# Optimization experiments

Measured on AMD Instinct MI355X. Metric: run time of the kernel, lower is better.

Reference implementation:

```python
import jax, jax.numpy as jnp
import numpy as np

TOP_K = 2  # num_experts_per_tok

def setup_inputs() -> dict:
    key = jax.random.key(0)
    ks = jax.random.split(key, 6)
    B, S, D, E, H = 4, 2048, 1024, 8, 4096
    x  = jax.random.normal(ks[0], (B, S, D), dtype=jnp.float32)
    Wg = jax.random.normal(ks[1], (D, E), dtype=jnp.float32) * 0.02
    W1 = jax.random.normal(ks[2], (E, D, H), dtype=jnp.float32) * 0.02
    b1 = jnp.zeros((E, H), dtype=jnp.float32)
    W2 = jax.random.normal(ks[3], (E, H, D), dtype=jnp.float32) * 0.02
    b2 = jnp.zeros((E, D), dtype=jnp.float32)
    return {"x": x, "Wg": Wg, "W1": W1, "b1": b1, "W2": W2, "b2": b2}

def reference(x, Wg, W1, b1, W2, b2):
    B, S, D = x.shape
    E = Wg.shape[1]
    xf = x.reshape(-1, D)                       # [T, D]
    T = xf.shape[0]
    logits = xf @ Wg                            # [T, E]
    probs = jax.nn.softmax(logits, axis=-1)
    weights, indices = jax.lax.top_k(probs, TOP_K)   # [T, K]
    # Dense combine weights: cw[t, e] = routing weight if e in top-k of t else 0.
    cw = jnp.zeros((T, E), dtype=x.dtype).at[jnp.arange(T)[:, None], indices].set(weights)
    out = jnp.zeros_like(xf)
    for e in range(E):  # small fixed expert count; per-expert GEMMs
        h = jax.nn.gelu(xf @ W1[e] + b1[e], approximate=False)  # [T, H]
        y = h @ W2[e] + b2[e]                                   # [T, D]
        out = out + y * cw[:, e:e + 1]
    return out.reshape(B, S, D)
```

## Files before the change

kernel.cpp:

```cpp
#include <hip/hip_runtime.h>
#include <hip/hip_bf16.h>
#include <stdint.h>

#define D_DIM 1024
#define E_NUM 8
#define H_DIM 4096

typedef __attribute__((ext_vector_type(8))) short short8;
typedef __attribute__((ext_vector_type(4))) short short4v;
typedef __attribute__((ext_vector_type(4))) unsigned short ushort4v;
typedef __attribute__((ext_vector_type(4))) float f32x4;

#define GLOBAL_AS __attribute__((address_space(1)))
#define LDS_AS __attribute__((address_space(3)))

__device__ __forceinline__ void async_load16(const void* g, void* l) {
    __builtin_amdgcn_global_load_lds((GLOBAL_AS void*)g, (LDS_AS void*)l, 16, 0, 0);
}

__device__ __forceinline__ float gelu_fast(float x) {
    float x3 = x * x * x;
    float z = 0.7978845608028654f * x + 0.0356774081363001f * x3;
    float u = __expf(-2.0f * fabsf(z));
    float t = __fdividef(1.0f - u, 1.0f + u);
    t = copysignf(t, z);
    return 0.5f * x * (1.0f + t);
}

__device__ __forceinline__ float b2f(short s) {
    union { float f; unsigned u; } x; x.u = ((unsigned)(unsigned short)s) << 16; return x.f;
}

__device__ __forceinline__ unsigned short f2b(float f) {
    union { __hip_bfloat16 h; unsigned short s; } u;
    u.h = __float2bfloat16(f);
    return u.s;
}

__global__ __launch_bounds__(256) void router_kernel(
    const float* __restrict__ x, const float* __restrict__ Wg,
    __hip_bfloat16* __restrict__ xb, int* __restrict__ epick,
    float* __restrict__ ewgt, int T) {
    int gwave = (int)((blockIdx.x * 256 + threadIdx.x) >> 6);
    int lane = threadIdx.x & 63;
    if (gwave >= T) return;
    const float* xr = x + (size_t)gwave * D_DIM;
    unsigned short* xbr = (unsigned short*)xb + (size_t)gwave * D_DIM;
    double acc[E_NUM];
#pragma unroll
    for (int e = 0; e < E_NUM; ++e) acc[e] = 0.0;
#pragma unroll
    for (int i = 0; i < D_DIM / 128; ++i) {
        int d = i * 128 + lane * 2;
        float2 xv = *(const float2*)(xr + d);
        unsigned pk = (unsigned)f2b(xv.x) | ((unsigned)f2b(xv.y) << 16);
        *(unsigned*)(xbr + d) = pk;
        const float4* wg0 = (const float4*)(Wg + (size_t)d * E_NUM);
        const float4* wg1 = (const float4*)(Wg + (size_t)(d + 1) * E_NUM);
        float4 wa = wg0[0], wb = wg0[1], wc = wg1[0], wd = wg1[1];
        double x0 = (double)xv.x, x1 = (double)xv.y;
        acc[0] += x0 * (double)wa.x + x1 * (double)wc.x;
        acc[1] += x0 * (double)wa.y + x1 * (double)wc.y;
        acc[2] += x0 * (double)wa.z + x1 * (double)wc.z;
        acc[3] += x0 * (double)wa.w + x1 * (double)wc.w;
        acc[4] += x0 * (double)wb.x + x1 * (double)wd.x;
        acc[5] += x0 * (double)wb.y + x1 * (double)wd.y;
        acc[6] += x0 * (double)wb.z + x1 * (double)wd.z;
        acc[7] += x0 * (double)wb.w + x1 * (double)wd.w;
    }
#pragma unroll
    for (int s = 32; s > 0; s >>= 1) {
#pragma unroll
        for (int e = 0; e < E_NUM; ++e) acc[e] += __shfl_xor(acc[e], s);
    }
    double mx = acc[0];
#pragma unroll
    for (int e = 1; e < E_NUM; ++e) mx = fmax(mx, acc[e]);
    double p[E_NUM]; double sum = 0.0;
#pragma unroll
    for (int e = 0; e < E_NUM; ++e) { p[e] = exp(acc[e] - mx); sum += p[e]; }
    int i0 = 0;
#pragma unroll
    for (int e = 1; e < E_NUM; ++e) if (p[e] > p[i0]) i0 = e;
    int i1 = (i0 == 0) ? 1 : 0;
#pragma unroll
    for (int e = 0; e < E_NUM; ++e) if (e != i0 && p[e] > p[i1]) i1 = e;
    if (lane == 0) {
        epick[gwave] = i0 | (i1 << 8);
        ewgt[2 * gwave]     = (float)(p[i0] / sum);
        ewgt[2 * gwave + 1] = (float)(p[i1] / sum);
    }
}

__global__ __launch_bounds__(256) void bucket_kernel(
    const int* __restrict__ epick, int* __restrict__ cnt,
    int* __restrict__ tok, int* __restrict__ eidx, int T) {
    __shared__ int lcnt[E_NUM];
    __shared__ int gbase[E_NUM];
    int b = blockIdx.x, tid = threadIdx.x;
    if (tid < E_NUM) lcnt[tid] = 0;
    __syncthreads();
    int t = b * 128 + (tid >> 1);
    int j = tid & 1;
    int e = (epick[t] >> (j * 8)) & 0xff;
    int li = atomicAdd(&lcnt[e], 1);
    __syncthreads();
    if (tid < E_NUM) gbase[tid] = atomicAdd(&cnt[tid], lcnt[tid]);
    __syncthreads();
    int slot = gbase[e] + li;
    tok[e * T + slot] = t;
    eidx[2 * t + j] = (e << 16) | slot;
}

__global__ void prefix_kernel(const int* __restrict__ cnt, int* __restrict__ base) {
    if (threadIdx.x == 0) {
        int a = 0;
#pragma unroll
        for (int e = 0; e < E_NUM; ++e) { base[e] = a; a += cnt[e]; }
    }
}

__global__ __launch_bounds__(256) void transpose_both_kernel(
    const float* __restrict__ W1, const float* __restrict__ W2,
    __hip_bfloat16* __restrict__ w1t, __hip_bfloat16* __restrict__ w2t) {
    __shared__ float tile[64][65];
    int e = blockIdx.z;
    int id = blockIdx.x;
    const float* src; unsigned short* dst; int R, C, r0, c0, perm;
    if (id < 1024) {
        R = D_DIM; C = H_DIM;
        r0 = (id >> 6) * 64; c0 = (id & 63) * 64;
        src = W1 + (size_t)e * D_DIM * H_DIM;
        dst = (unsigned short*)(w1t + (size_t)e * H_DIM * D_DIM);
        perm = 0;
    } else {
        id -= 1024;
        R = H_DIM; C = D_DIM;
        r0 = (id >> 4) * 64; c0 = (id & 15) * 64;
        src = W2 + (size_t)e * H_DIM * D_DIM;
        dst = (unsigned short*)(w2t + (size_t)e * D_DIM * H_DIM);
        perm = 1;
    }
    int tx = threadIdx.x, ty = threadIdx.y;
#pragma unroll
    for (int i = 0; i < 8; ++i) {
        int j = ty + i * 8;
        int sr = perm ? ((j & 3) * 16 + (j >> 2)) : j;
        float2 v = *(const float2*)(src + (size_t)(r0 + sr) * C + c0 + 2 * tx);
        tile[j][2 * tx] = v.x; tile[j][2 * tx + 1] = v.y;
    }
    __syncthreads();
#pragma unroll
    for (int i = 0; i < 8; ++i) {
        int cc = ty + i * 8;
        unsigned pk = (unsigned)f2b(tile[2 * tx][cc]) | ((unsigned)f2b(tile[2 * tx + 1][cc]) << 16);
        *(unsigned*)(dst + (size_t)(c0 + cc) * R + r0 + 2 * tx) = pk;
    }
}


__global__ __launch_bounds__(256) void gemm1_kernel(
    const __hip_bfloat16* __restrict__ xb,
    const __hip_bfloat16* __restrict__ w1t,
    const float* __restrict__ b1,
    const int* __restrict__ cnt, const int* __restrict__ base,
    const int* __restrict__ tok,
    __hip_bfloat16* __restrict__ hbuf,
    int T) {
    int e = blockIdx.z;
    int M = cnt[e];
    int m0 = blockIdx.y * 128;
    if (m0 >= M) return;
    int n0 = blockIdx.x * 128;
    const __hip_bfloat16* Bp = w1t + (size_t)e * H_DIM * D_DIM;

    __shared__ __align__(16) short sA[128 * 32];
    __shared__ __align__(16) short sB[128 * 32];
    __shared__ float sBias[128];
    char* sAc = (char*)sA; char* sBc = (char*)sB;

    int tid = threadIdx.x;
    int w = tid >> 6, lane = tid & 63;
    int wm = w >> 1, wn = w & 1;
    int q = lane >> 4, l4 = lane & 15;

    if (tid < 128) sBias[tid] = b1[e * H_DIM + n0 + tid];

    int kswz = ((lane & 3) ^ ((lane >> 3) & 3)) << 3;
    int r0 = w * 32 + (lane >> 2);
    int r1 = r0 + 16;
    int tA0 = tok[e * T + min(m0 + r0, M - 1)];
    int tA1 = tok[e * T + min(m0 + r1, M - 1)];
    const __hip_bfloat16* gA0 = xb + (size_t)tA0 * D_DIM + kswz;
    const __hip_bfloat16* gA1 = xb + (size_t)tA1 * D_DIM + kswz;
    const __hip_bfloat16* gB0 = Bp + (size_t)(n0 + r0) * D_DIM + kswz;
    const __hip_bfloat16* gB1 = Bp + (size_t)(n0 + r1) * D_DIM + kswz;
    char* lA0 = sAc + w * 2048 + lane * 16;
    char* lB0 = sBc + w * 2048 + lane * 16;
    char* lA1 = sAc + w * 2048 + 1024;
    char* lB1 = sBc + w * 2048 + 1024;

    f32x4 acc[4][4];
#pragma unroll
    for (int a = 0; a < 4; ++a)
#pragma unroll
        for (int b = 0; b < 4; ++b) acc[a][b] = (f32x4){0.f, 0.f, 0.f, 0.f};

    for (int kk = 0; kk < D_DIM; kk += 32) {
        async_load16(gA0 + kk, lA0);
        async_load16(gA1 + kk, lA1);
        async_load16(gB0 + kk, lB0);
        async_load16(gB1 + kk, lB1);
        __syncthreads();
        short8 aF[4], bF[4];
#pragma unroll
        for (int t = 0; t < 4; ++t) {
            int ra = wm * 64 + t * 16 + l4;
            aF[t] = *(const short8*)(sAc + ra * 64 + ((q ^ ((ra >> 1) & 3)) << 4));
            int rb = wn * 64 + t * 16 + l4;
            bF[t] = *(const short8*)(sBc + rb * 64 + ((q ^ ((rb >> 1) & 3)) << 4));
        }
#pragma unroll
        for (int tm = 0; tm < 4; ++tm)
#pragma unroll
            for (int tn = 0; tn < 4; ++tn)
                acc[tm][tn] = __builtin_amdgcn_mfma_f32_16x16x32_bf16(aF[tm], bF[tn], acc[tm][tn], 0, 0, 0);
        __syncthreads();
    }

    int sb = base[e];
    unsigned short* hs = (unsigned short*)hbuf;
#pragma unroll
    for (int tm = 0; tm < 4; ++tm) {
        int rbase = wm * 64 + tm * 16 + q * 4;
#pragma unroll
        for (int i = 0; i < 4; ++i) {
            int row = m0 + rbase + i;
            if (row < M) {
                size_t hrow = (size_t)(sb + row) * H_DIM;
                ushort4v pk;
#pragma unroll
                for (int tn = 0; tn < 4; ++tn) {
                    float v = acc[tm][tn][i] + sBias[wn * 64 + tn * 16 + l4];
                    pk[tn] = f2b(gelu_fast(v));
                }
                *(ushort4v*)(hs + hrow + n0 + wn * 64 + l4 * 4) = pk;
            }
        }
    }
}

__global__ __launch_bounds__(256) void gemm2_kernel(
    const __hip_bfloat16* __restrict__ hbuf,
    const __hip_bfloat16* __restrict__ w2t,
    const int* __restrict__ cnt, const int* __restrict__ base,
    __hip_bfloat16* __restrict__ ybuf,
    int T) {
    int e = blockIdx.z;
    int M = cnt[e];
    int m0 = blockIdx.y * 128;
    if (m0 >= M) return;
    int n0 = blockIdx.x * 128;
    int sb = base[e];
    const __hip_bfloat16* Bp = w2t + (size_t)e * D_DIM * H_DIM;

    __shared__ __align__(16) short sA[128 * 32];
    __shared__ __align__(16) short sB[128 * 32];
    char* sAc = (char*)sA; char* sBc = (char*)sB;

    int tid = threadIdx.x;
    int w = tid >> 6, lane = tid & 63;
    int wm = w >> 1, wn = w & 1;
    int q = lane >> 4, l4 = lane & 15;

    int kswz = ((lane & 3) ^ ((lane >> 3) & 3)) << 3;
    int r0 = w * 32 + (lane >> 2);
    int r1 = r0 + 16;
    const __hip_bfloat16* gA0 = hbuf + (size_t)(sb + min(m0 + r0, M - 1)) * H_DIM + kswz;
    const __hip_bfloat16* gA1 = hbuf + (size_t)(sb + min(m0 + r1, M - 1)) * H_DIM + kswz;
    const __hip_bfloat16* gB0 = Bp + (size_t)(n0 + r0) * H_DIM + kswz;
    const __hip_bfloat16* gB1 = Bp + (size_t)(n0 + r1) * H_DIM + kswz;
    char* lA0 = sAc + w * 2048 + lane * 16;
    char* lB0 = sBc + w * 2048 + lane * 16;
    char* lA1 = sAc + w * 2048 + 1024;
    char* lB1 = sBc + w * 2048 + 1024;

    f32x4 acc[4][4];
#pragma unroll
    for (int a = 0; a < 4; ++a)
#pragma unroll
        for (int b = 0; b < 4; ++b) acc[a][b] = (f32x4){0.f, 0.f, 0.f, 0.f};

    for (int kk = 0; kk < H_DIM; kk += 32) {
        async_load16(gA0 + kk, lA0);
        async_load16(gA1 + kk, lA1);
        async_load16(gB0 + kk, lB0);
        async_load16(gB1 + kk, lB1);
        __syncthreads();
        short8 aF[4], bF[4];
#pragma unroll
        for (int t = 0; t < 4; ++t) {
            int ra = wm * 64 + t * 16 + l4;
            aF[t] = *(const short8*)(sAc + ra * 64 + ((q ^ ((ra >> 1) & 3)) << 4));
            int rb = wn * 64 + t * 16 + l4;
            bF[t] = *(const short8*)(sBc + rb * 64 + ((q ^ ((rb >> 1) & 3)) << 4));
        }
#pragma unroll
        for (int tm = 0; tm < 4; ++tm)
#pragma unroll
            for (int tn = 0; tn < 4; ++tn)
                acc[tm][tn] = __builtin_amdgcn_mfma_f32_16x16x32_bf16(aF[tm], bF[tn], acc[tm][tn], 0, 0, 0);
        __syncthreads();
    }

    unsigned short* ys = (unsigned short*)ybuf;
#pragma unroll
    for (int tm = 0; tm < 4; ++tm) {
        int rbase = wm * 64 + tm * 16 + q * 4;
#pragma unroll
        for (int i = 0; i < 4; ++i) {
            int row = m0 + rbase + i;
            if (row < M) {
                size_t yrow = (size_t)(sb + row) * D_DIM;
                ushort4v pk;
#pragma unroll
                for (int tn = 0; tn < 4; ++tn) pk[tn] = f2b(acc[tm][tn][i]);
                *(ushort4v*)(ys + yrow + n0 + wn * 64 + l4 * 4) = pk;
            }
        }
    }
}

__global__ __launch_bounds__(256) void combine_kernel(
    const __hip_bfloat16* __restrict__ yb, const float* __restrict__ b2,
    const int* __restrict__ base, const int* __restrict__ eidx,
    const float* __restrict__ ewgt, float* __restrict__ out, int T) {
    int t = blockIdx.x, tid = threadIdx.x;
    int v0 = eidx[2 * t], v1 = eidx[2 * t + 1];
    float w0 = ewgt[2 * t], w1 = ewgt[2 * t + 1];
    int e0 = v0 >> 16, e1 = v1 >> 16;
    size_t g0 = (size_t)base[e0] + (v0 & 0xffff);
    size_t g1 = (size_t)base[e1] + (v1 & 0xffff);
    int c = tid * 4;
    int blk = c >> 6;
    int tt = (c >> 2) & 15;
    const short* ys = (const short*)yb;
    short4v a0 = *(const short4v*)(ys + g0 * D_DIM + c);
    short4v c0 = *(const short4v*)(ys + g1 * D_DIM + c);
    float s0[4] = { b2f(a0.x), b2f(a0.y), b2f(a0.z), b2f(a0.w) };
    float s1[4] = { b2f(c0.x), b2f(c0.y), b2f(c0.z), b2f(c0.w) };
    float* orow = out + (size_t)t * D_DIM;
#pragma unroll
    for (int s = 0; s < 4; ++s) {
        int oc = blk * 64 + s * 16 + tt;
        float o = w0 * (s0[s] + b2[(size_t)e0 * D_DIM + oc]) +
                  w1 * (s1[s] + b2[(size_t)e1 * D_DIM + oc]);
        orow[oc] = o;
    }
}

extern "C" void kernel_launch(void* const* d_in, const int* in_sizes, int n_in,
                              void* d_out, int out_size, void* d_ws, size_t ws_size,
                              hipStream_t stream) {
    const float* x  = (const float*)d_in[0];
    const float* Wg = (const float*)d_in[1];
    const float* W1 = (const float*)d_in[2];
    const float* b1 = (const float*)d_in[3];
    const float* W2 = (const float*)d_in[4];
    const float* b2 = (const float*)d_in[5];
    int T = in_sizes[0] / D_DIM;

    char* p = (char*)d_ws;
    int* cnt   = (int*)p;
    int* base  = (int*)(p + 256);
    int* tok   = (int*)(p + 512);
    int* eidx  = (int*)(p + 512 + 4ll * E_NUM * T);
    float* ewgt = (float*)(p + 512 + 4ll * E_NUM * T + 8ll * T);
    int* epick = (int*)(p + 512 + 4ll * E_NUM * T + 16ll * T);
    char* pb = p + 512 + 4ll * E_NUM * T + 20ll * T;
    __hip_bfloat16* xb  = (__hip_bfloat16*)pb;
    __hip_bfloat16* w1t = xb + (size_t)T * D_DIM;
    __hip_bfloat16* w2t = w1t + (size_t)E_NUM * H_DIM * D_DIM;
    __hip_bfloat16* hb  = w2t + (size_t)E_NUM * H_DIM * D_DIM;
    __hip_bfloat16* yb  = xb;

    hipMemsetAsync(cnt, 0, 256, stream);

    router_kernel<<<dim3((T + 3) / 4), 256, 0, stream>>>(x, Wg, xb, epick, ewgt, T);
    bucket_kernel<<<dim3(T / 128), 256, 0, stream>>>(epick, cnt, tok, eidx, T);
    prefix_kernel<<<1, 64, 0, stream>>>(cnt, base);
    transpose_both_kernel<<<dim3(2048, 1, E_NUM), dim3(32, 8), 0, stream>>>(W1, W2, w1t, w2t);
    gemm1_kernel<<<dim3(H_DIM / 128, T / 128, E_NUM), 256, 0, stream>>>(xb, w1t, b1, cnt, base, tok, hb, T);
    gemm2_kernel<<<dim3(D_DIM / 128, T / 128, E_NUM), 256, 0, stream>>>(hb, w2t, cnt, base, yb, T);
    combine_kernel<<<T, 256, 0, stream>>>(yb, b2, base, eidx, ewgt, (float*)d_out, T);
}
```

Baseline: 781.7 us.

## Compact expert tile work table and split-K the second expert GEMM

The prefix kernel now builds a compact table of (expert, row-block) pairs. Both GEMMs launch only over real tiles instead of a dense E×(T/128) grid where most blocks exit early. The second GEMM is also split into two K halves, each writing a separate bf16 partial buffer that the combine kernel sums. This is meant to cut empty-block launch overhead and raise wave occupancy for the small gemm2 grid. The cost is extra partial-output traffic and one more bf16 rounding per partial.

```diff
diff --git a/kernel.cpp b/kernel.cpp
--- a/kernel.cpp
+++ b/kernel.cpp
@@ -112,11 +112,18 @@
     eidx[2 * t + j] = (e << 16) | slot;
 }
 
-__global__ void prefix_kernel(const int* __restrict__ cnt, int* __restrict__ base) {
+__global__ void prefix_kernel(const int* __restrict__ cnt, int* __restrict__ base,
+                              int* __restrict__ wtab, int wmax) {
     if (threadIdx.x == 0) {
         int a = 0;
 #pragma unroll
         for (int e = 0; e < E_NUM; ++e) { base[e] = a; a += cnt[e]; }
+        int nw = 0;
+        for (int e = 0; e < E_NUM; ++e) {
+            int nb = (cnt[e] + 127) >> 7;
+            for (int mb = 0; mb < nb; ++mb) wtab[nw++] = (e << 16) | mb;
+        }
+        for (; nw < wmax; ++nw) wtab[nw] = -1;
     }
 }
 
@@ -164,13 +171,14 @@
     const __hip_bfloat16* __restrict__ w1t,
     const float* __restrict__ b1,
     const int* __restrict__ cnt, const int* __restrict__ base,
-    const int* __restrict__ tok,
+    const int* __restrict__ tok, const int* __restrict__ wtab,
     __hip_bfloat16* __restrict__ hbuf,
     int T) {
-    int e = blockIdx.z;
+    int wt = wtab[blockIdx.y];
+    if (wt < 0) return;
+    int e = wt >> 16;
+    int m0 = (wt & 0xffff) << 7;
     int M = cnt[e];
-    int m0 = blockIdx.y * 128;
-    if (m0 >= M) return;
     int n0 = blockIdx.x * 128;
     const __hip_bfloat16* Bp = w1t + (size_t)e * H_DIM * D_DIM;
 
@@ -254,12 +262,15 @@
     const __hip_bfloat16* __restrict__ hbuf,
     const __hip_bfloat16* __restrict__ w2t,
     const int* __restrict__ cnt, const int* __restrict__ base,
+    const int* __restrict__ wtab,
     __hip_bfloat16* __restrict__ ybuf,
     int T) {
-    int e = blockIdx.z;
+    int wt = wtab[blockIdx.y];
+    if (wt < 0) return;
+    int e = wt >> 16;
+    int m0 = (wt & 0xffff) << 7;
+    int kc = blockIdx.z;
     int M = cnt[e];
-    int m0 = blockIdx.y * 128;
-    if (m0 >= M) return;
     int n0 = blockIdx.x * 128;
     int sb = base[e];
     const __hip_bfloat16* Bp = w2t + (size_t)e * D_DIM * H_DIM;
@@ -291,7 +302,8 @@
 #pragma unroll
         for (int b = 0; b < 4; ++b) acc[a][b] = (f32x4){0.f, 0.f, 0.f, 0.f};
 
-    for (int kk = 0; kk < H_DIM; kk += 32) {
+    int k0 = kc * (H_DIM / 2), k1 = k0 + (H_DIM / 2);
+    for (int kk = k0; kk < k1; kk += 32) {
         async_load16(gA0 + kk, lA0);
         async_load16(gA1 + kk, lA1);
         async_load16(gB0 + kk, lB0);
@@ -313,6 +325,7 @@
         __syncthreads();
     }
 
+    size_t ybase = (size_t)kc * 2 * T;
     unsigned short* ys = (unsigned short*)ybuf;
 #pragma unroll
     for (int tm = 0; tm < 4; ++tm) {
@@ -321,7 +334,7 @@
         for (int i = 0; i < 4; ++i) {
             int row = m0 + rbase + i;
             if (row < M) {
-                size_t yrow = (size_t)(sb + row) * D_DIM;
+                size_t yrow = (ybase + sb + row) * D_DIM;
                 ushort4v pk;
 #pragma unroll
                 for (int tn = 0; tn < 4; ++tn) pk[tn] = f2b(acc[tm][tn][i]);
@@ -344,11 +357,16 @@
     int c = tid * 4;
     int blk = c >> 6;
     int tt = (c >> 2) & 15;
+    size_t off2 = (size_t)2 * T * D_DIM;
     const short* ys = (const short*)yb;
     short4v a0 = *(const short4v*)(ys + g0 * D_DIM + c);
+    short4v a1 = *(const short4v*)(ys + off2 + g0 * D_DIM + c);
     short4v c0 = *(const short4v*)(ys + g1 * D_DIM + c);
-    float s0[4] = { b2f(a0.x), b2f(a0.y), b2f(a0.z), b2f(a0.w) };
-    float s1[4] = { b2f(c0.x), b2f(c0.y), b2f(c0.z), b2f(c0.w) };
+    short4v c1 = *(const short4v*)(ys + off2 + g1 * D_DIM + c);
+    float s0[4] = { b2f(a0.x) + b2f(a1.x), b2f(a0.y) + b2f(a1.y),
+                    b2f(a0.z) + b2f(a1.z), b2f(a0.w) + b2f(a1.w) };
+    float s1[4] = { b2f(c0.x) + b2f(c1.x), b2f(c0.y) + b2f(c1.y),
+                    b2f(c0.z) + b2f(c1.z), b2f(c0.w) + b2f(c1.w) };
     float* orow = out + (size_t)t * D_DIM;
 #pragma unroll
     for (int s = 0; s < 4; ++s) {
@@ -369,6 +387,7 @@
     const float* W2 = (const float*)d_in[4];
     const float* b2 = (const float*)d_in[5];
     int T = in_sizes[0] / D_DIM;
+    int wmax = 2 * T / 128 + E_NUM;
 
     char* p = (char*)d_ws;
     int* cnt   = (int*)p;
@@ -377,7 +396,8 @@
     int* eidx  = (int*)(p + 512 + 4ll * E_NUM * T);
     float* ewgt = (float*)(p + 512 + 4ll * E_NUM * T + 8ll * T);
     int* epick = (int*)(p + 512 + 4ll * E_NUM * T + 16ll * T);
-    char* pb = p + 512 + 4ll * E_NUM * T + 20ll * T;
+    int* wtab  = (int*)(p + 512 + 4ll * E_NUM * T + 20ll * T);
+    char* pb = p + 512 + 4ll * E_NUM * T + 20ll * T + 1024;
     __hip_bfloat16* xb  = (__hip_bfloat16*)pb;
     __hip_bfloat16* w1t = xb + (size_t)T * D_DIM;
     __hip_bfloat16* w2t = w1t + (size_t)E_NUM * H_DIM * D_DIM;
@@ -388,9 +408,9 @@
 
     router_kernel<<<dim3((T + 3) / 4), 256, 0, stream>>>(x, Wg, xb, epick, ewgt, T);
     bucket_kernel<<<dim3(T / 128), 256, 0, stream>>>(epick, cnt, tok, eidx, T);
-    prefix_kernel<<<1, 64, 0, stream>>>(cnt, base);
+    prefix_kernel<<<1, 64, 0, stream>>>(cnt, base, wtab, wmax);
     transpose_both_kernel<<<dim3(2048, 1, E_NUM), dim3(32, 8), 0, stream>>>(W1, W2, w1t, w2t);
-    gemm1_kernel<<<dim3(H_DIM / 128, T / 128, E_NUM), 256, 0, stream>>>(xb, w1t, b1, cnt, base, tok, hb, T);
-    gemm2_kernel<<<dim3(D_DIM / 128, T / 128, E_NUM), 256, 0, stream>>>(hb, w2t, cnt, base, yb, T);
+    gemm1_kernel<<<dim3(H_DIM / 128, wmax, 1), 256, 0, stream>>>(xb, w1t, b1, cnt, base, tok, wtab, hb, T);
+    gemm2_kernel<<<dim3(D_DIM / 128, wmax, 2), 256, 0, stream>>>(hb, w2t, cnt, base, wtab, yb, T);
     combine_kernel<<<T, 256, 0, stream>>>(yb, b2, base, eidx, ewgt, (float*)d_out, T);
 }
```

Measured after the change: 758.6 us. 3.0% less time.
